# Kernel tuning notes

Measured on AMD Instinct MI355X. Metric: run time of the kernel, lower is better.

The kernel has to match this reference:

```python
import jax, jax.numpy as jnp
import numpy as np

N = 100000      # nodes
E = 1600000     # edges (avg degree 16)
D_IN = 256
H = 128         # hidden_dim
D_OUT = 64
BN_EPS = 1e-5


def setup_inputs() -> dict:
    key = jax.random.key(0)
    ks = jax.random.split(key, 16)
    s = 0.05  # small init scale
    x = jax.random.normal(ks[0], (N, D_IN), jnp.float32)
    edge_index = jax.random.randint(ks[1], (2, E), 0, N)
    inp = {
        "x": x,
        "edge_index": edge_index,
        "w_in": jax.random.normal(ks[2], (D_IN, H), jnp.float32) * s,
        "b_in": jnp.zeros((H,), jnp.float32),
        # SAGEConv layer 1: lin_l (neighbors, with bias) + lin_r (self, no bias)
        "w_l1": jax.random.normal(ks[3], (H, H), jnp.float32) * s,
        "b_l1": jnp.zeros((H,), jnp.float32),
        "w_r1": jax.random.normal(ks[4], (H, H), jnp.float32) * s,
        "g1": jnp.ones((H,), jnp.float32),
        "be1": jnp.zeros((H,), jnp.float32),
        # SAGEConv layer 2
        "w_l2": jax.random.normal(ks[5], (H, H), jnp.float32) * s,
        "b_l2": jnp.zeros((H,), jnp.float32),
        "w_r2": jax.random.normal(ks[6], (H, H), jnp.float32) * s,
        "g2": jnp.ones((H,), jnp.float32),
        "be2": jnp.zeros((H,), jnp.float32),
        "w_out": jax.random.normal(ks[7], (H, D_OUT), jnp.float32) * s,
        "b_out": jnp.zeros((D_OUT,), jnp.float32),
    }
    return inp


def _sage_conv(x, src, dst, w_l, b_l, w_r):
    # gather messages from source nodes, mean-aggregate at target nodes
    msgs = x[src]                                           # [E, H]
    agg = jax.ops.segment_sum(msgs, dst, num_segments=N)    # [N, H]
    deg = jax.ops.segment_sum(jnp.ones((src.shape[0], 1), x.dtype), dst,
                              num_segments=N)               # [N, 1]
    mean = agg / jnp.maximum(deg, 1.0)
    return mean @ w_l + b_l + x @ w_r


def _bn_eval(h, gamma, beta):
    # BatchNorm1d in eval mode: running_mean=0, running_var=1
    return h * (gamma / jnp.sqrt(1.0 + BN_EPS)) + beta


def reference(x, edge_index, w_in, b_in,
              w_l1, b_l1, w_r1, g1, be1,
              w_l2, b_l2, w_r2, g2, be2,
              w_out, b_out):
    src, dst = edge_index[0], edge_index[1]
    h = jax.nn.relu(x @ w_in + b_in)                         # [N, H]
    h = _sage_conv(h, src, dst, w_l1, b_l1, w_r1)
    h = jax.nn.relu(_bn_eval(h, g1, be1))                    # dropout off (eval)
    h = _sage_conv(h, src, dst, w_l2, b_l2, w_r2)
    h = jax.nn.relu(_bn_eval(h, g2, be2))
    return h @ w_out + b_out                                 # [N, D_OUT]
```

## Files before the change

kernel.cpp:

```cpp
#include <hip/hip_runtime.h>

#define DIN 256
#define H   128
#define DOUT 64

#define EPI_RELU 0
#define EPI_BN   1
#define EPI_NONE 2

#define BKT_SHIFT 7
#define BKT_NODES 128
#define BKT_CAP   4096

typedef __attribute__((ext_vector_type(8))) short bf16x8;
typedef __attribute__((ext_vector_type(4))) float f32x4;

__device__ inline unsigned short f2bf(float f) {
  union { float f; unsigned u; } v; v.f = f;
  unsigned u = v.u;
  u += 0x7FFFu + ((u >> 16) & 1u);
  return (unsigned short)(u >> 16);
}
__device__ inline float bf2f(unsigned u16) {
  union { unsigned u; float f; } v; v.u = u16 << 16;
  return v.f;
}

#define FILL_TPB 1024
#define FILL_EPT 16
#define FILL_EPB (FILL_TPB * FILL_EPT)

__global__ __launch_bounds__(FILL_TPB) void bucket_fill(
    const int* __restrict__ src, const int* __restrict__ dst,
    int* __restrict__ bcur, unsigned* __restrict__ bedges,
    int nbkt, int e) {
  __shared__ int hist[1024];
  int tid = threadIdx.x;
  int base = blockIdx.x * FILL_EPB;
  for (int i = tid; i < nbkt; i += FILL_TPB) hist[i] = 0;
  __syncthreads();

  int es[FILL_EPT], ed[FILL_EPT];
#pragma unroll
  for (int j = 0; j < FILL_EPT; ++j) {
    int i = base + j * FILL_TPB + tid;
    if (i < e) {
      es[j] = src[i];
      ed[j] = dst[i];
      atomicAdd(&hist[ed[j] >> BKT_SHIFT], 1);
    } else {
      es[j] = -1; ed[j] = 0;
    }
  }
  __syncthreads();
  for (int b = tid; b < nbkt; b += FILL_TPB) {
    int cnt = hist[b];
    hist[b] = cnt ? atomicAdd(&bcur[b], cnt) : 0;
  }
  __syncthreads();
#pragma unroll
  for (int j = 0; j < FILL_EPT; ++j) {
    if (es[j] >= 0) {
      int b = ed[j] >> BKT_SHIFT;
      int p = atomicAdd(&hist[b], 1);
      if (p < BKT_CAP)
        bedges[(size_t)b * BKT_CAP + p] =
            (unsigned)es[j] | ((unsigned)(ed[j] & (BKT_NODES - 1)) << 17);
    }
  }
}

__global__ __launch_bounds__(256) void bucket_sort(
    const int* __restrict__ bcur, const unsigned* __restrict__ bedges,
    int* __restrict__ csr, int* __restrict__ row_beg, int* __restrict__ deg,
    int n) {
  __shared__ unsigned rec[BKT_CAP];
  __shared__ int srcs[BKT_CAP];
  __shared__ int hist[BKT_NODES];
  __shared__ int cursor[BKT_NODES];
  int tid = threadIdx.x;
  int b = blockIdx.x;
  int cnt = bcur[b];
  if (cnt > BKT_CAP) cnt = BKT_CAP;
  const unsigned* eb = bedges + (size_t)b * BKT_CAP;

  if (tid < BKT_NODES) hist[tid] = 0;
  __syncthreads();
  for (int i = tid; i < cnt; i += 256) {
    unsigned r = eb[i];
    rec[i] = r;
    atomicAdd(&hist[(r >> 17) & 127], 1);
  }
  __syncthreads();
  int myc = (tid < BKT_NODES) ? hist[tid] : 0;
#pragma unroll
  for (int off = 1; off < BKT_NODES; off <<= 1) {
    int v = 0;
    if (tid < BKT_NODES && tid >= off) v = hist[tid - off];
    __syncthreads();
    if (tid < BKT_NODES) hist[tid] += v;
    __syncthreads();
  }
  if (tid < BKT_NODES) {
    int start = hist[tid] - myc;
    cursor[tid] = start;
    int node = b * BKT_NODES + tid;
    if (node < n) {
      row_beg[node] = b * BKT_CAP + start;
      deg[node] = myc;
    }
  }
  __syncthreads();
  for (int i = tid; i < cnt; i += 256) {
    unsigned r = rec[i];
    int p = atomicAdd(&cursor[(r >> 17) & 127], 1);
    srcs[p] = (int)(r & 0x1FFFFu);
  }
  __syncthreads();
  for (int i = tid; i < cnt; i += 256)
    csr[(size_t)b * BKT_CAP + i] = srcs[i];
}

__global__ __launch_bounds__(256) void agg_kernel(const unsigned* __restrict__ h,
                                                  const int* __restrict__ row_beg,
                                                  const int* __restrict__ deg,
                                                  const int* __restrict__ csr,
                                                  unsigned* __restrict__ mean, int n) {
  int node = (int)((blockIdx.x * blockDim.x + threadIdx.x) >> 6);
  if (node >= n) return;
  int lane = threadIdx.x & 63;
  int beg = row_beg[node], d = deg[node];
  float ax = 0.f, ay = 0.f;
  for (int j0 = 0; j0 < d; j0 += 64) {
    int cnt = min(64, d - j0);
    int li = j0 + (lane < cnt ? lane : cnt - 1);
    int sv = csr[beg + li];
    int j = 0;
    for (; j + 8 <= cnt; j += 8) {
      unsigned v[8];
#pragma unroll
      for (int q = 0; q < 8; ++q) {
        int s = __shfl(sv, j + q);
        v[q] = h[(size_t)s * (H / 2) + lane];
      }
#pragma unroll
      for (int q = 0; q < 8; ++q) {
        ax += bf2f(v[q] & 0xffffu);
        ay += bf2f(v[q] >> 16);
      }
    }
    for (; j < cnt; ++j) {
      int s = __shfl(sv, j);
      unsigned v = h[(size_t)s * (H / 2) + lane];
      ax += bf2f(v & 0xffffu);
      ay += bf2f(v >> 16);
    }
  }
  float invd = 1.f / (float)(d > 0 ? d : 1);
  mean[(size_t)node * (H / 2) + lane] =
      (unsigned)f2bf(ax * invd) | ((unsigned)f2bf(ay * invd) << 16);
}

__global__ __launch_bounds__(256) void prep_w(
    const float* __restrict__ w_in, const float* __restrict__ w_l1,
    const float* __restrict__ w_r1, const float* __restrict__ w_l2,
    const float* __restrict__ w_r2, const float* __restrict__ w_out,
    unsigned short* __restrict__ t_in, unsigned short* __restrict__ t_l1,
    unsigned short* __restrict__ t_r1, unsigned short* __restrict__ t_l2,
    unsigned short* __restrict__ t_r2, unsigned short* __restrict__ t_out) {
  int i = blockIdx.x * 256 + threadIdx.x;
  const float* s; unsigned short* d; int K, M, off;
  if (i < 32768)       { s = w_in;  d = t_in;  K = 256; M = 128; off = i; }
  else if (i < 49152)  { s = w_l1;  d = t_l1;  K = 128; M = 128; off = i - 32768; }
  else if (i < 65536)  { s = w_r1;  d = t_r1;  K = 128; M = 128; off = i - 49152; }
  else if (i < 81920)  { s = w_l2;  d = t_l2;  K = 128; M = 128; off = i - 65536; }
  else if (i < 98304)  { s = w_r2;  d = t_r2;  K = 128; M = 128; off = i - 81920; }
  else if (i < 106496) { s = w_out; d = t_out; K = 128; M = 64;  off = i - 98304; }
  else return;
  int m = off / K, k = off % K;
  d[off] = f2bf(s[(size_t)k * M + m]);
}

template <int NPH, int KOFF2, int AKA, int AKW, int M, int EPI, bool AFP32, bool OUTF32>
__global__ __launch_bounds__(256) void gemm_mfma(
    const void* __restrict__ A1, const void* __restrict__ A2,
    const unsigned short* __restrict__ W1, const unsigned short* __restrict__ W2,
    const float* __restrict__ bias, const float* __restrict__ gamma,
    const float* __restrict__ beta, void* __restrict__ Cv, int n) {
  constexpr int NT = M / 16;
  __shared__ __align__(16) unsigned short As[64 * 128];
  __shared__ __align__(16) unsigned short Bs[M * 128];

  int tid = threadIdx.x, lane = tid & 63, wave = tid >> 6;
  int m16 = lane & 15, quad = lane >> 4;
  int row0 = blockIdx.x * 64;
  int sr = lane >> 4;
  int sc = lane & 15;

  f32x4 acc[NT];
#pragma unroll
  for (int t = 0; t < NT; ++t) acc[t] = (f32x4){0.f, 0.f, 0.f, 0.f};

#pragma unroll
  for (int ph = 0; ph < NPH; ++ph) {
    const void* A_ = ph ? A2 : A1;
    const unsigned short* W = ph ? W2 : W1;
    const int koff = ph ? KOFF2 : 0;
    if (ph) __syncthreads();

    if constexpr (!AFP32) {
#pragma unroll
      for (int g = 0; g < 4; ++g) {
        int lr = wave * 16 + g * 4 + sr;
        int grow = row0 + lr; if (grow >= n) grow = n - 1;
        uint4 v = *(const uint4*)((const unsigned short*)A_ +
                                  (size_t)grow * AKA + koff + sc * 8);
        *(uint4*)&As[lr * 128 + ((sc + lr) & 15) * 8] = v;
      }
    } else {
      int sr2 = lane >> 5;
      int c32 = lane & 31;
#pragma unroll
      for (int g = 0; g < 8; ++g) {
        int lr = wave * 16 + g * 2 + sr2;
        int grow = row0 + lr; if (grow >= n) grow = n - 1;
        float4 v = *(const float4*)((const float*)A_ +
                                    (size_t)grow * AKA + koff + c32 * 4);
        unsigned p0 = (unsigned)f2bf(v.x) | ((unsigned)f2bf(v.y) << 16);
        unsigned p1 = (unsigned)f2bf(v.z) | ((unsigned)f2bf(v.w) << 16);
        int ch = c32 >> 1;
        *(uint2*)&As[lr * 128 + ((ch + lr) & 15) * 8 + (c32 & 1) * 4] =
            make_uint2(p0, p1);
      }
    }
#pragma unroll
    for (int g = 0; g < M / 16; ++g) {
      int br = wave * (M / 4) + g * 4 + sr;
      uint4 v = *(const uint4*)(W + (size_t)br * AKW + koff + sc * 8);
      *(uint4*)&Bs[br * 128 + ((sc + br) & 15) * 8] = v;
    }
    __syncthreads();

    int lrme = wave * 16 + m16;
#pragma unroll
    for (int kt = 0; kt < 4; ++kt) {
      int ch = kt * 4 + quad;
      bf16x8 a = *(const bf16x8*)&As[lrme * 128 + ((ch + lrme) & 15) * 8];
#pragma unroll
      for (int t = 0; t < NT; ++t) {
        int brow = t * 16 + m16;
        bf16x8 b = *(const bf16x8*)&Bs[brow * 128 + ((ch + brow) & 15) * 8];
        acc[t] = __builtin_amdgcn_mfma_f32_16x16x32_bf16(a, b, acc[t], 0, 0, 0);
      }
    }
  }

  const float inv_std = rsqrtf(1.f + 1e-5f);
#pragma unroll
  for (int t = 0; t < NT; ++t) {
    int col = t * 16 + m16;
    float bv = bias[col];
    float sc2 = 1.f, bt2 = 0.f;
    if constexpr (EPI == EPI_BN) {
      sc2 = gamma[col] * inv_std;
      bt2 = beta[col];
    }
#pragma unroll
    for (int r = 0; r < 4; ++r) {
      int row = row0 + wave * 16 + quad * 4 + r;
      if (row < n) {
        float v = acc[t][r] + bv;
        if constexpr (EPI == EPI_BN) v = fmaxf(v * sc2 + bt2, 0.f);
        else if constexpr (EPI == EPI_RELU) v = fmaxf(v, 0.f);
        if constexpr (OUTF32)
          ((float*)Cv)[(size_t)row * M + col] = v;
        else
          ((unsigned short*)Cv)[(size_t)row * M + col] = f2bf(v);
      }
    }
  }
}

extern "C" void kernel_launch(void* const* d_in, const int* in_sizes, int n_in,
                              void* d_out, int out_size, void* d_ws, size_t ws_size,
                              hipStream_t stream) {
  const float* x     = (const float*)d_in[0];
  const int*   ei    = (const int*)d_in[1];
  const float* w_in  = (const float*)d_in[2];
  const float* b_in  = (const float*)d_in[3];
  const float* w_l1  = (const float*)d_in[4];
  const float* b_l1  = (const float*)d_in[5];
  const float* w_r1  = (const float*)d_in[6];
  const float* g1    = (const float*)d_in[7];
  const float* be1   = (const float*)d_in[8];
  const float* w_l2  = (const float*)d_in[9];
  const float* b_l2  = (const float*)d_in[10];
  const float* w_r2  = (const float*)d_in[11];
  const float* g2    = (const float*)d_in[12];
  const float* be2   = (const float*)d_in[13];
  const float* w_out = (const float*)d_in[14];
  const float* b_out = (const float*)d_in[15];
  float* out = (float*)d_out;

  int N = in_sizes[0] / DIN;
  int E = in_sizes[1] / 2;
  const int* src = ei;
  const int* dst = ei + E;
  int nbkt = (N + BKT_NODES - 1) / BKT_NODES;

  char* ws = (char*)d_ws;
  size_t off = 0;
  auto alloc = [&](size_t bytes) -> char* {
    char* p = ws + off;
    off += (bytes + 255) & ~(size_t)255;
    return p;
  };
  unsigned short* buf0 = (unsigned short*)alloc((size_t)N * H * 2);
  unsigned short* buf1 = (unsigned short*)alloc((size_t)N * H * 2);
  unsigned short* buf2 = (unsigned short*)alloc((size_t)N * H * 2);
  int* bcur        = (int*)alloc((size_t)nbkt * 4);
  unsigned* bedges = (unsigned*)alloc((size_t)nbkt * BKT_CAP * 4);
  int* csr         = (int*)alloc((size_t)nbkt * BKT_CAP * 4);
  int* row_beg     = (int*)alloc((size_t)N * 4);
  int* deg         = (int*)alloc((size_t)N * 4);
  unsigned short* t_in  = (unsigned short*)alloc(32768 * 2);
  unsigned short* t_l1  = (unsigned short*)alloc(16384 * 2);
  unsigned short* t_r1  = (unsigned short*)alloc(16384 * 2);
  unsigned short* t_l2  = (unsigned short*)alloc(16384 * 2);
  unsigned short* t_r2  = (unsigned short*)alloc(16384 * 2);
  unsigned short* t_out = (unsigned short*)alloc(8192 * 2);
  (void)ws_size;

  hipMemsetAsync(bcur, 0, (size_t)nbkt * 4, stream);
  bucket_fill<<<(E + FILL_EPB - 1) / FILL_EPB, FILL_TPB, 0, stream>>>(
      src, dst, bcur, bedges, nbkt, E);
  bucket_sort<<<nbkt, 256, 0, stream>>>(bcur, bedges, csr, row_beg, deg, N);
  prep_w<<<(106496 + 255) / 256, 256, 0, stream>>>(
      w_in, w_l1, w_r1, w_l2, w_r2, w_out, t_in, t_l1, t_r1, t_l2, t_r2, t_out);

  int gblocks = (N + 63) / 64;
  int ablocks = (N + 3) / 4;

  gemm_mfma<2, 128, 256, 256, 128, EPI_RELU, true, false><<<gblocks, 256, 0, stream>>>(
      x, x, t_in, t_in, b_in, nullptr, nullptr, buf0, N);
  agg_kernel<<<ablocks, 256, 0, stream>>>((const unsigned*)buf0, row_beg, deg,
                                          csr, (unsigned*)buf1, N);
  gemm_mfma<2, 0, 128, 128, 128, EPI_BN, false, false><<<gblocks, 256, 0, stream>>>(
      buf1, buf0, t_l1, t_r1, b_l1, g1, be1, buf2, N);
  agg_kernel<<<ablocks, 256, 0, stream>>>((const unsigned*)buf2, row_beg, deg,
                                          csr, (unsigned*)buf0, N);
  gemm_mfma<2, 0, 128, 128, 128, EPI_BN, false, false><<<gblocks, 256, 0, stream>>>(
      buf0, buf2, t_l2, t_r2, b_l2, g2, be2, buf1, N);
  gemm_mfma<1, 0, 128, 128, 64, EPI_NONE, false, true><<<gblocks, 256, 0, stream>>>(
      buf1, buf1, t_out, t_out, b_out, nullptr, nullptr, out, N);
}
```

Baseline: 429.6 us.

## Restructure aggregation: 16 lanes per node with uint4 gathers and padded CSR

The aggregation kernel now handles four nodes per wavefront, with 16 lanes per node each loading a 16-byte uint4 (eight bf16 values) instead of one 32-bit word per lane. The bucket sort pads each node's edge list to a multiple of four and zero-fills a 16-entry tail, so neighbor indices can be read as aligned int4 vectors without bounds checks. Out-of-range slots are masked by a zero weight in the FMA. Row start and degree are packed into a single int2. This aims to cut per-edge instruction and shuffle overhead and widen memory transactions, at the cost of extra CSR storage and wasted gathers on padded slots.

```diff
diff --git a/kernel.cpp b/kernel.cpp
--- a/kernel.cpp
+++ b/kernel.cpp
@@ -11,6 +11,7 @@
 #define BKT_SHIFT 7
 #define BKT_NODES 128
 #define BKT_CAP   4096
+#define CSR_CAP   4608
 
 typedef __attribute__((ext_vector_type(8))) short bf16x8;
 typedef __attribute__((ext_vector_type(4))) float f32x4;
@@ -72,12 +73,12 @@
 
 __global__ __launch_bounds__(256) void bucket_sort(
     const int* __restrict__ bcur, const unsigned* __restrict__ bedges,
-    int* __restrict__ csr, int* __restrict__ row_beg, int* __restrict__ deg,
-    int n) {
+    int* __restrict__ csr, int2* __restrict__ rowdeg, int n) {
   __shared__ unsigned rec[BKT_CAP];
-  __shared__ int srcs[BKT_CAP];
+  __shared__ int srcs[CSR_CAP];
   __shared__ int hist[BKT_NODES];
   __shared__ int cursor[BKT_NODES];
+  __shared__ int s_total;
   int tid = threadIdx.x;
   int b = blockIdx.x;
   int cnt = bcur[b];
@@ -93,6 +94,9 @@
   }
   __syncthreads();
   int myc = (tid < BKT_NODES) ? hist[tid] : 0;
+  int myc4 = (myc + 3) & ~3;
+  if (tid < BKT_NODES) hist[tid] = myc4;
+  __syncthreads();
 #pragma unroll
   for (int off = 1; off < BKT_NODES; off <<= 1) {
     int v = 0;
@@ -101,14 +105,13 @@
     if (tid < BKT_NODES) hist[tid] += v;
     __syncthreads();
   }
+  int start = 0;
   if (tid < BKT_NODES) {
-    int start = hist[tid] - myc;
+    start = hist[tid] - myc4;
     cursor[tid] = start;
     int node = b * BKT_NODES + tid;
-    if (node < n) {
-      row_beg[node] = b * BKT_CAP + start;
-      deg[node] = myc;
-    }
+    if (node < n) rowdeg[node] = make_int2(b * CSR_CAP + start, myc);
+    if (tid == BKT_NODES - 1) s_total = hist[tid];
   }
   __syncthreads();
   for (int i = tid; i < cnt; i += 256) {
@@ -116,49 +119,70 @@
     int p = atomicAdd(&cursor[(r >> 17) & 127], 1);
     srcs[p] = (int)(r & 0x1FFFFu);
   }
-  __syncthreads();
-  for (int i = tid; i < cnt; i += 256)
-    csr[(size_t)b * BKT_CAP + i] = srcs[i];
-}
-
-__global__ __launch_bounds__(256) void agg_kernel(const unsigned* __restrict__ h,
-                                                  const int* __restrict__ row_beg,
-                                                  const int* __restrict__ deg,
-                                                  const int* __restrict__ csr,
-                                                  unsigned* __restrict__ mean, int n) {
-  int node = (int)((blockIdx.x * blockDim.x + threadIdx.x) >> 6);
-  if (node >= n) return;
+  if (tid < BKT_NODES) {
+    for (int g = start + myc; g < start + myc4; ++g) srcs[g] = 0;
+  }
+  __syncthreads();
+  int total = s_total;
+  if (tid < 16 && total + tid < CSR_CAP) srcs[total + tid] = 0;
+  __syncthreads();
+  int tot16 = total + 16;
+  if (tot16 > CSR_CAP) tot16 = CSR_CAP;
+  for (int i = tid; i < tot16; i += 256)
+    csr[(size_t)b * CSR_CAP + i] = srcs[i];
+}
+
+__global__ __launch_bounds__(256) void agg_kernel(
+    const unsigned* __restrict__ h, const int2* __restrict__ rowdeg,
+    const int* __restrict__ csr, unsigned* __restrict__ mean, int n) {
+  int wid = (blockIdx.x * 256 + threadIdx.x) >> 6;
   int lane = threadIdx.x & 63;
-  int beg = row_beg[node], d = deg[node];
-  float ax = 0.f, ay = 0.f;
-  for (int j0 = 0; j0 < d; j0 += 64) {
-    int cnt = min(64, d - j0);
-    int li = j0 + (lane < cnt ? lane : cnt - 1);
-    int sv = csr[beg + li];
-    int j = 0;
-    for (; j + 8 <= cnt; j += 8) {
-      unsigned v[8];
-#pragma unroll
-      for (int q = 0; q < 8; ++q) {
-        int s = __shfl(sv, j + q);
-        v[q] = h[(size_t)s * (H / 2) + lane];
-      }
-#pragma unroll
-      for (int q = 0; q < 8; ++q) {
-        ax += bf2f(v[q] & 0xffffu);
-        ay += bf2f(v[q] >> 16);
-      }
-    }
-    for (; j < cnt; ++j) {
-      int s = __shfl(sv, j);
-      unsigned v = h[(size_t)s * (H / 2) + lane];
-      ax += bf2f(v & 0xffffu);
-      ay += bf2f(v >> 16);
-    }
-  }
-  float invd = 1.f / (float)(d > 0 ? d : 1);
-  mean[(size_t)node * (H / 2) + lane] =
-      (unsigned)f2bf(ax * invd) | ((unsigned)f2bf(ay * invd) << 16);
+  int grp = lane >> 4;
+  int c = lane & 15;
+  int node = wid * 4 + grp;
+  bool valid = node < n;
+  if (!valid) node = 0;
+  int2 rd = rowdeg[node];
+  int beg = rd.x, d = rd.y;
+
+  const uint4* hv = (const uint4*)h;
+  float a[8];
+#pragma unroll
+  for (int k = 0; k < 8; ++k) a[k] = 0.f;
+
+  for (int j0 = 0; j0 < d; j0 += 16) {
+    int rem = d - j0;
+    const int4* sp = (const int4*)(csr + beg + j0);
+    int sv[16];
+    *(int4*)&sv[0]  = sp[0];
+    *(int4*)&sv[4]  = sp[1];
+    *(int4*)&sv[8]  = sp[2];
+    *(int4*)&sv[12] = sp[3];
+#pragma unroll
+    for (int jj = 0; jj < 16; ++jj) {
+      float w = (jj < rem) ? 1.f : 0.f;
+      uint4 v = hv[(unsigned)(sv[jj] * 16 + c)];
+#pragma unroll
+      for (int k = 0; k < 4; ++k) {
+        unsigned u = ((const unsigned*)&v)[k];
+        union { unsigned u; float f; } lo, hi;
+        lo.u = u << 16;
+        hi.u = u & 0xffff0000u;
+        a[2 * k]     = fmaf(w, lo.f, a[2 * k]);
+        a[2 * k + 1] = fmaf(w, hi.f, a[2 * k + 1]);
+      }
+    }
+  }
+
+  if (valid) {
+    float invd = 1.f / (float)(d > 0 ? d : 1);
+    uint4 o;
+    o.x = (unsigned)f2bf(a[0] * invd) | ((unsigned)f2bf(a[1] * invd) << 16);
+    o.y = (unsigned)f2bf(a[2] * invd) | ((unsigned)f2bf(a[3] * invd) << 16);
+    o.z = (unsigned)f2bf(a[4] * invd) | ((unsigned)f2bf(a[5] * invd) << 16);
+    o.w = (unsigned)f2bf(a[6] * invd) | ((unsigned)f2bf(a[7] * invd) << 16);
+    ((uint4*)mean)[(unsigned)(node * 16 + c)] = o;
+  }
 }
 
 __global__ __launch_bounds__(256) void prep_w(
@@ -320,9 +344,8 @@
   unsigned short* buf2 = (unsigned short*)alloc((size_t)N * H * 2);
   int* bcur        = (int*)alloc((size_t)nbkt * 4);
   unsigned* bedges = (unsigned*)alloc((size_t)nbkt * BKT_CAP * 4);
-  int* csr         = (int*)alloc((size_t)nbkt * BKT_CAP * 4);
-  int* row_beg     = (int*)alloc((size_t)N * 4);
-  int* deg         = (int*)alloc((size_t)N * 4);
+  int* csr         = (int*)alloc((size_t)nbkt * CSR_CAP * 4);
+  int2* rowdeg     = (int2*)alloc((size_t)N * 8);
   unsigned short* t_in  = (unsigned short*)alloc(32768 * 2);
   unsigned short* t_l1  = (unsigned short*)alloc(16384 * 2);
   unsigned short* t_r1  = (unsigned short*)alloc(16384 * 2);
@@ -334,20 +357,20 @@
   hipMemsetAsync(bcur, 0, (size_t)nbkt * 4, stream);
   bucket_fill<<<(E + FILL_EPB - 1) / FILL_EPB, FILL_TPB, 0, stream>>>(
       src, dst, bcur, bedges, nbkt, E);
-  bucket_sort<<<nbkt, 256, 0, stream>>>(bcur, bedges, csr, row_beg, deg, N);
+  bucket_sort<<<nbkt, 256, 0, stream>>>(bcur, bedges, csr, rowdeg, N);
   prep_w<<<(106496 + 255) / 256, 256, 0, stream>>>(
       w_in, w_l1, w_r1, w_l2, w_r2, w_out, t_in, t_l1, t_r1, t_l2, t_r2, t_out);
 
   int gblocks = (N + 63) / 64;
-  int ablocks = (N + 3) / 4;
+  int ablocks = (N + 15) / 16;
 
   gemm_mfma<2, 128, 256, 256, 128, EPI_RELU, true, false><<<gblocks, 256, 0, stream>>>(
       x, x, t_in, t_in, b_in, nullptr, nullptr, buf0, N);
-  agg_kernel<<<ablocks, 256, 0, stream>>>((const unsigned*)buf0, row_beg, deg,
+  agg_kernel<<<ablocks, 256, 0, stream>>>((const unsigned*)buf0, rowdeg,
                                           csr, (unsigned*)buf1, N);
   gemm_mfma<2, 0, 128, 128, 128, EPI_BN, false, false><<<gblocks, 256, 0, stream>>>(
       buf1, buf0, t_l1, t_r1, b_l1, g1, be1, buf2, N);
-  agg_kernel<<<ablocks, 256, 0, stream>>>((const unsigned*)buf2, row_beg, deg,
+  agg_kernel<<<ablocks, 256, 0, stream>>>((const unsigned*)buf2, rowdeg,
                                           csr, (unsigned*)buf0, N);
   gemm_mfma<2, 0, 128, 128, 128, EPI_BN, false, false><<<gblocks, 256, 0, stream>>>(
       buf0, buf2, t_l2, t_r2, b_l2, g2, be2, buf1, N);
```

Result: no change. 425.7 us (-0.9%).
